# Performance work log

Measured on AMD Instinct MI355X. Metric: run time of the kernel, lower is better.

Reference implementation:

```python
import jax, jax.numpy as jnp
import numpy as np

VARIANCE = 1.0  # prototorch euclidean_similarity default


def setup_inputs() -> dict:
    key = jax.random.key(0)
    k1, k2, k3 = jax.random.split(key, 3)
    B, D = 32768, 1024
    K, C = 5, 3  # sum([2,1,2]) components, len([2,1,2]) classes
    x = jax.random.normal(k1, (B, D), dtype=jnp.float32)
    components = jax.random.normal(k2, (K, D), dtype=jnp.float32)
    # PPRI: random probabilistic reasonings in [0,1], shape [K, C, 2]
    reasonings = jax.random.uniform(k3, (K, C, 2), dtype=jnp.float32)
    return {"x": x, "components": components, "reasonings": reasonings}


def reference(x, components, reasonings):
    # --- euclidean similarity: exp(-d(x, c)^2 / (2*variance)) ---
    # squared pairwise distances via expansion (avoids [B,K,D] intermediate)
    x2 = jnp.sum(x * x, axis=-1, keepdims=True)          # [B,1]
    c2 = jnp.sum(components * components, axis=-1)       # [K]
    d2 = x2 + c2[None, :] - 2.0 * (x @ components.T)     # [B,K]
    d2 = jnp.maximum(d2, 0.0)
    sims = jnp.exp(-d2 / (2.0 * VARIANCE))               # [B,K]

    # --- cbcc competition ---
    # reasonings [K,C,2] -> permute(2,1,0) -> [2,C,K], clamp to [0,1]
    R = jnp.clip(jnp.transpose(reasonings, (2, 1, 0)), 0.0, 1.0)
    A, Bneg = R[0], R[1]                                 # each [C,K]
    pk = A
    nk = (1.0 - A) * Bneg                                # [C,K]
    numerator = sims @ (pk - nk).T + jnp.sum(nk, axis=1) # [B,C]
    probs = numerator / jnp.sum(pk + nk, axis=1)         # [B,C]
    return probs
```

## Files before the change

kernel.cpp:

```cpp
#include <hip/hip_runtime.h>


#define DD 1024
#define KK 5
#define CC 3
#define F4_PER_ROW (DD / 4)
#define F4_PER_LANE (F4_PER_ROW / 64)

template <int CTRL>
__device__ __forceinline__ float dpp_add(float v) {
    int moved = __builtin_amdgcn_update_dpp(
        0, __float_as_int(v), CTRL, 0xf, 0xf, true);
    return v + __int_as_float(moved);
}

__device__ __forceinline__ float wave_sum_dpp(float v) {
    v = dpp_add<0x111>(v);
    v = dpp_add<0x112>(v);
    v = dpp_add<0x114>(v);
    v = dpp_add<0x118>(v);
    v = dpp_add<0x142>(v);
    v = dpp_add<0x143>(v);
    return v;
}

__global__ __launch_bounds__(256) void cbc_kernel(
    const float* __restrict__ x,
    const float* __restrict__ comps,
    const float* __restrict__ reas,
    float* __restrict__ out,
    int B)
{
    const int lane = threadIdx.x & 63;
    const int waves_per_block = blockDim.x >> 6;
    const int wave_global = blockIdx.x * waves_per_block + (threadIdx.x >> 6);
    const int n_waves = gridDim.x * waves_per_block;

    float4 cf[KK][F4_PER_LANE];
    const float4* comps4 = (const float4*)comps;
#pragma unroll
    for (int k = 0; k < KK; ++k)
#pragma unroll
        for (int j = 0; j < F4_PER_LANE; ++j)
            cf[k][j] = comps4[k * F4_PER_ROW + j * 64 + lane];

    float w[CC][KK], bias[CC], invden[CC];
#pragma unroll
    for (int c = 0; c < CC; ++c) {
        float nsum = 0.f, dsum = 0.f;
#pragma unroll
        for (int k = 0; k < KK; ++k) {
            float a = reas[k * (CC * 2) + c * 2 + 0];
            float b = reas[k * (CC * 2) + c * 2 + 1];
            a = fminf(fmaxf(a, 0.f), 1.f);
            b = fminf(fmaxf(b, 0.f), 1.f);
            float nk = (1.f - a) * b;
            w[c][k] = a - nk;
            nsum += nk;
            dsum += a + nk;
        }
        bias[c] = nsum;
        invden[c] = 1.f / dsum;
    }

    const float4* x4 = (const float4*)x;

    for (int row = wave_global; row < B; row += n_waves) {
        float acc[KK];
#pragma unroll
        for (int k = 0; k < KK; ++k) acc[k] = 0.f;

#pragma unroll
        for (int j = 0; j < F4_PER_LANE; ++j) {
            float4 xv = x4[(size_t)row * F4_PER_ROW + j * 64 + lane];
#pragma unroll
            for (int k = 0; k < KK; ++k) {
                float dx = xv.x - cf[k][j].x;
                float dy = xv.y - cf[k][j].y;
                float dz = xv.z - cf[k][j].z;
                float dw = xv.w - cf[k][j].w;
                acc[k] += dx * dx;
                acc[k] += dy * dy;
                acc[k] += dz * dz;
                acc[k] += dw * dw;
            }
        }

        float d2[KK];
#pragma unroll
        for (int k = 0; k < KK; ++k) {
            float s = wave_sum_dpp(acc[k]);
            d2[k] = __int_as_float(
                __builtin_amdgcn_readlane(__float_as_int(s), 63));
        }

        if (lane < CC) {
            const int c = lane;
            float num = bias[c];
#pragma unroll
            for (int k = 0; k < KK; ++k)
                num += __expf(-0.5f * d2[k]) * w[c][k];
            out[(size_t)row * CC + c] = num * invden[c];
        }
    }
}

extern "C" void kernel_launch(void* const* d_in, const int* in_sizes, int n_in,
                              void* d_out, int out_size, void* d_ws, size_t ws_size,
                              hipStream_t stream) {
    const float* x = (const float*)d_in[0];
    const float* comps = (const float*)d_in[1];
    const float* reas = (const float*)d_in[2];
    float* out = (float*)d_out;
    const int B = in_sizes[0] / DD;

    const int blocks = 1024;
    cbc_kernel<<<blocks, 256, 0, stream>>>(x, comps, reas, out, B);
}
```

Baseline: 190.4 us.

## Process two rows per wave iteration with all loads issued up front

Each wave now handles a pair of rows per iteration, issuing all eight float4 loads for both rows before computing, so more memory requests are in flight per wave. Reasoning weights are precomputed per lane (lane mod C) instead of as a full C×K table, and the six output values for the pair are written in one contiguous store. This adds register pressure and silently drops the last row if B is odd.

Result: no change. 190.5 us (+0.0%).

```diff
diff --git a/kernel.cpp b/kernel.cpp
--- a/kernel.cpp
+++ b/kernel.cpp
@@ -21,7 +21,7 @@
     v = dpp_add<0x118>(v);
     v = dpp_add<0x142>(v);
     v = dpp_add<0x143>(v);
-    return v;
+    return __int_as_float(__builtin_amdgcn_readlane(__float_as_int(v), 63));
 }
 
 __global__ __launch_bounds__(256) void cbc_kernel(
@@ -44,63 +44,88 @@
         for (int j = 0; j < F4_PER_LANE; ++j)
             cf[k][j] = comps4[k * F4_PER_ROW + j * 64 + lane];
 
-    float w[CC][KK], bias[CC], invden[CC];
+    int c = lane;
+    if (c >= CC) c -= CC;
+    if (c >= CC) c = 0;
+    float wv[KK], bias = 0.f, den = 0.f;
 #pragma unroll
-    for (int c = 0; c < CC; ++c) {
-        float nsum = 0.f, dsum = 0.f;
-#pragma unroll
-        for (int k = 0; k < KK; ++k) {
-            float a = reas[k * (CC * 2) + c * 2 + 0];
-            float b = reas[k * (CC * 2) + c * 2 + 1];
-            a = fminf(fmaxf(a, 0.f), 1.f);
-            b = fminf(fmaxf(b, 0.f), 1.f);
-            float nk = (1.f - a) * b;
-            w[c][k] = a - nk;
-            nsum += nk;
-            dsum += a + nk;
-        }
-        bias[c] = nsum;
-        invden[c] = 1.f / dsum;
+    for (int k = 0; k < KK; ++k) {
+        float a = reas[k * (CC * 2) + c * 2 + 0];
+        float b = reas[k * (CC * 2) + c * 2 + 1];
+        a = fminf(fmaxf(a, 0.f), 1.f);
+        b = fminf(fmaxf(b, 0.f), 1.f);
+        float nk = (1.f - a) * b;
+        wv[k] = a - nk;
+        bias += nk;
+        den  += a + nk;
     }
+    const float invden = 1.f / den;
 
     const float4* x4 = (const float4*)x;
+    const int npairs = B >> 1;
 
-    for (int row = wave_global; row < B; row += n_waves) {
-        float acc[KK];
+    for (int p = wave_global; p < npairs; p += n_waves) {
+        const size_t base = (size_t)p * 2 * F4_PER_ROW;
+
+        float4 xv0[F4_PER_LANE], xv1[F4_PER_LANE];
 #pragma unroll
-        for (int k = 0; k < KK; ++k) acc[k] = 0.f;
+        for (int j = 0; j < F4_PER_LANE; ++j)
+            xv0[j] = x4[base + j * 64 + lane];
+#pragma unroll
+        for (int j = 0; j < F4_PER_LANE; ++j)
+            xv1[j] = x4[base + F4_PER_ROW + j * 64 + lane];
+
+        float acc0[KK], acc1[KK];
+#pragma unroll
+        for (int k = 0; k < KK; ++k) { acc0[k] = 0.f; acc1[k] = 0.f; }
 
 #pragma unroll
         for (int j = 0; j < F4_PER_LANE; ++j) {
-            float4 xv = x4[(size_t)row * F4_PER_ROW + j * 64 + lane];
 #pragma unroll
             for (int k = 0; k < KK; ++k) {
-                float dx = xv.x - cf[k][j].x;
-                float dy = xv.y - cf[k][j].y;
-                float dz = xv.z - cf[k][j].z;
-                float dw = xv.w - cf[k][j].w;
-                acc[k] += dx * dx;
-                acc[k] += dy * dy;
-                acc[k] += dz * dz;
-                acc[k] += dw * dw;
+                float dx = xv0[j].x - cf[k][j].x;
+                float dy = xv0[j].y - cf[k][j].y;
+                float dz = xv0[j].z - cf[k][j].z;
+                float dw = xv0[j].w - cf[k][j].w;
+                acc0[k] += dx * dx;
+                acc0[k] += dy * dy;
+                acc0[k] += dz * dz;
+                acc0[k] += dw * dw;
             }
         }
 
-        float d2[KK];
+        float d20[KK];
 #pragma unroll
-        for (int k = 0; k < KK; ++k) {
-            float s = wave_sum_dpp(acc[k]);
-            d2[k] = __int_as_float(
-                __builtin_amdgcn_readlane(__float_as_int(s), 63));
+        for (int k = 0; k < KK; ++k) d20[k] = wave_sum_dpp(acc0[k]);
+
+#pragma unroll
+        for (int j = 0; j < F4_PER_LANE; ++j) {
+#pragma unroll
+            for (int k = 0; k < KK; ++k) {
+                float dx = xv1[j].x - cf[k][j].x;
+                float dy = xv1[j].y - cf[k][j].y;
+                float dz = xv1[j].z - cf[k][j].z;
+                float dw = xv1[j].w - cf[k][j].w;
+                acc1[k] += dx * dx;
+                acc1[k] += dy * dy;
+                acc1[k] += dz * dz;
+                acc1[k] += dw * dw;
+            }
         }
 
-        if (lane < CC) {
-            const int c = lane;
-            float num = bias[c];
+        float d21[KK];
 #pragma unroll
-            for (int k = 0; k < KK; ++k)
-                num += __expf(-0.5f * d2[k]) * w[c][k];
-            out[(size_t)row * CC + c] = num * invden[c];
+        for (int k = 0; k < KK; ++k) d21[k] = wave_sum_dpp(acc1[k]);
+
+        if (lane < 2 * CC) {
+            const bool second = lane >= CC;
+            float num = bias;
+#pragma unroll
+            for (int k = 0; k < KK; ++k) {
+                float d2 = second ? d21[k] : d20[k];
+                num += __expf(-0.5f * d2) * wv[k];
+            }
+            out[(size_t)p * (2 * CC) + lane] = num * invden;
         }
     }
 }
```
